# Kernel optimization log

Hardware: AMD Instinct MI355X
Metric: run time of the kernel (lower is better)

The kernel has to match this reference:

```python
import jax, jax.numpy as jnp
import numpy as np

FILTERS = [1, 3, 7, 9]
BN_EPS = 1e-5


def _conv1d(x, w, b):
    # x: [B, C, L], w: [O, I, F] (torch Conv1d layout), 'same' padding for odd F
    pad = (w.shape[-1] - 1) // 2
    y = jax.lax.conv_general_dilated(
        x, w, window_strides=(1,), padding=[(pad, pad)],
        dimension_numbers=("NCH", "OIH", "NCH"))
    return y + b[None, :, None]


def _bn_elu(x, gamma, beta):
    # BatchNorm1d in training mode: biased batch stats over (batch, length)
    m = jnp.mean(x, axis=(0, 2), keepdims=True)
    v = jnp.var(x, axis=(0, 2), keepdims=True)
    xn = (x - m) * jax.lax.rsqrt(v + BN_EPS)
    return jax.nn.elu(xn * gamma[None, :, None] + beta[None, :, None])


def setup_inputs() -> dict:
    key = jax.random.key(0)
    ks = jax.random.split(key, 32)
    b, h, l, lk, dk = 8, 8, 1024, 1024, 64
    inp = {
        "Q": jax.random.normal(ks[0], (b, h, l, dk), jnp.float32),
        "K": jax.random.normal(ks[1], (b, h, lk, dk), jnp.float32),
        "V": jax.random.normal(ks[2], (b, h, lk, dk), jnp.float32),
        "W_pq": jax.random.normal(ks[3], (1, dk), jnp.float32) * 0.1,
        "W_bq": jax.random.normal(ks[4], (dk, 1), jnp.float32) * 0.1,
        "W_bk": jax.random.normal(ks[5], (dk, 1), jnp.float32) * 0.1,
        "bn_g": jax.random.uniform(ks[6], (h,), jnp.float32, 0.5, 1.5),
        "bn_b": jax.random.normal(ks[7], (h,), jnp.float32) * 0.1,
        "attn_mask": jnp.ones((1,), dtype=bool),
    }
    for i, f in enumerate(FILTERS):
        s = 1.0 / np.sqrt(h * f)
        inp[f"cq_w{i}"] = jax.random.normal(ks[8 + i], (h, h, f), jnp.float32) * s
        inp[f"cq_b{i}"] = jax.random.normal(ks[12 + i], (h,), jnp.float32) * 0.05
        inp[f"ck_w{i}"] = jax.random.normal(ks[16 + i], (h, h, f), jnp.float32) * s
        inp[f"ck_b{i}"] = jax.random.normal(ks[20 + i], (h,), jnp.float32) * 0.05
    return inp


def reference(Q, K, V, W_pq, W_bq, W_bk,
              cq_w0, cq_b0, cq_w1, cq_b1, cq_w2, cq_b2, cq_w3, cq_b3,
              ck_w0, ck_b0, ck_w1, ck_b1, ck_w2, ck_b2, ck_w3, ck_b3,
              bn_g, bn_b, attn_mask):
    b, h, l, dk = Q.shape
    lk = K.shape[2]
    nf = len(FILTERS)
    # proj_q applied to BOTH Q and K (proj_k is dead in the original code)
    q = jnp.einsum("bhld,d->bhl", Q, W_pq[0])  # [b,h,l]
    k = jnp.einsum("bhld,d->bhl", K, W_pq[0])  # [b,h,lk]
    cq = [(cq_w0, cq_b0), (cq_w1, cq_b1), (cq_w2, cq_b2), (cq_w3, cq_b3)]
    ck = [(ck_w0, ck_b0), (ck_w1, ck_b1), (ck_w2, ck_b2), (ck_w3, ck_b3)]
    Q_l = [_bn_elu(_conv1d(q, w, bb), bn_g, bn_b) for w, bb in cq]
    K_l = [_bn_elu(_conv1d(k, w, bb), bn_g, bn_b) for w, bb in ck]
    # replicate torch.cat(dim=0) + reshape(b,h,nf*len) flat-order semantics
    Q_p = jnp.concatenate(Q_l, axis=0).reshape(b, h, nf * l)    # [b,h,4l]
    K_p = jnp.concatenate(K_l, axis=0).reshape(b, h, nf * lk)   # [b,h,4lk]
    Qt = jax.lax.top_k(Q_p, l)[0]                               # [b,h,l]
    Km = jnp.mean(K_p.reshape(b, h, nf, lk), axis=2)            # [b,h,lk]
    Kt = jax.lax.top_k(Km, lk)[0]                               # descending sort
    Qb = Qt[..., None] * W_bq[:, 0]                             # [b,h,l,dk]
    Kb = Kt[..., None] * W_bk[:, 0]                             # [b,h,lk,dk]
    scores = jnp.einsum("bhqd,bhkd->bhqk", Qb, Kb) / np.float32(np.sqrt(dk))
    attn = jax.nn.softmax(scores, axis=-1)
    context = jnp.einsum("bhqk,bhkd->bhqd", attn, V)
    return context, attn
```

## Files before the change

### kernel.cpp

```cpp
#include <hip/hip_runtime.h>
#include <hip/hip_bf16.h>
#include <math.h>

namespace {
constexpr int PROJ_OFF = 0;
constexpr int CONV_OFF = 131072;
constexpr int PS_OFF   = 655360;
constexpr int PSS_OFF  = 657408;
constexpr int QT_OFF   = 659456;
constexpr int KT_OFF   = 724992;

typedef short bf16x8 __attribute__((ext_vector_type(8)));
typedef float f32x4 __attribute__((ext_vector_type(4)));

union BF8 {
  bf16x8 v;
  short s[8];
};

__global__ __launch_bounds__(256) void proj_kernel(
    const float* __restrict__ Q, const float* __restrict__ K,
    const float* __restrict__ Wpq, float* __restrict__ proj) {
  __shared__ float wsh[64];
  const int tid = threadIdx.x;
  if (tid < 64) wsh[tid] = Wpq[tid];
  __syncthreads();
  const int row = blockIdx.x * 256 + tid;
  const float* src = (row < 65536) ? (Q + (size_t)row * 64)
                                   : (K + (size_t)(row - 65536) * 64);
  float acc = 0.f;
#pragma unroll
  for (int j = 0; j < 16; ++j) {
    const float4 v = *(const float4*)(src + j * 4);
    acc = fmaf(v.x, wsh[j * 4 + 0], acc);
    acc = fmaf(v.y, wsh[j * 4 + 1], acc);
    acc = fmaf(v.z, wsh[j * 4 + 2], acc);
    acc = fmaf(v.w, wsh[j * 4 + 3], acc);
  }
  proj[row] = acc;
}

template <int F>
__device__ void conv_body(const float* __restrict__ xs,
                          const float* __restrict__ wsm,
                          const float* __restrict__ bsm,
                          float* __restrict__ outp, int tid, int lq,
                          float accs[8]) {
  constexpr int pad = (F - 1) / 2;
#pragma unroll
  for (int j = 0; j < 8; ++j) {
    float acc = bsm[j];
#pragma unroll
    for (int c = 0; c < 8; ++c) {
      const float* xrow = &xs[c * 264 + tid + 4 - pad];
      const float* wrow = &wsm[(j * 8 + c) * F];
#pragma unroll
      for (int f = 0; f < F; ++f) acc = fmaf(xrow[f], wrow[f], acc);
    }
    outp[j * 1024 + lq * 256 + tid] = acc;
    accs[j] = acc;
  }
}

__global__ __launch_bounds__(256) void conv_kernel(
    const float* __restrict__ proj,
    const float* __restrict__ wq0, const float* __restrict__ bq0,
    const float* __restrict__ wq1, const float* __restrict__ bq1,
    const float* __restrict__ wq2, const float* __restrict__ bq2,
    const float* __restrict__ wq3, const float* __restrict__ bq3,
    const float* __restrict__ wk0, const float* __restrict__ bk0,
    const float* __restrict__ wk1, const float* __restrict__ bk1,
    const float* __restrict__ wk2, const float* __restrict__ bk2,
    const float* __restrict__ wk3, const float* __restrict__ bk3,
    float* __restrict__ conv, float* __restrict__ psum,
    float* __restrict__ psumsq) {
  __shared__ float xs[8 * 264];
  __shared__ float wsm[8 * 8 * 9];
  __shared__ float bsm[8];
  __shared__ float redS[8][4], redSS[8][4];
  const int tid = threadIdx.x;
  const int blk = blockIdx.x;
  const int path = blk >> 7, fi = (blk >> 5) & 3, bb = (blk >> 2) & 7;
  const int lq = blk & 3;
  const int F = (0x9731 >> (fi * 4)) & 0xF;
  const float* wp;
  const float* bp;
  if (path == 0) {
    wp = fi == 0 ? wq0 : fi == 1 ? wq1 : fi == 2 ? wq2 : wq3;
    bp = fi == 0 ? bq0 : fi == 1 ? bq1 : fi == 2 ? bq2 : bq3;
  } else {
    wp = fi == 0 ? wk0 : fi == 1 ? wk1 : fi == 2 ? wk2 : wk3;
    bp = fi == 0 ? bk0 : fi == 1 ? bk1 : fi == 2 ? bk2 : bk3;
  }
  const float* pb = proj + path * 65536 + bb * 8192;
  for (int e = tid; e < 8 * 264; e += 256) {
    const int c = e / 264, pos = e - c * 264;
    const int gl = lq * 256 + pos - 4;
    xs[e] = (gl >= 0 && gl < 1024) ? pb[c * 1024 + gl] : 0.f;
  }
  for (int e = tid; e < 64 * F; e += 256) wsm[e] = wp[e];
  if (tid < 8) bsm[tid] = bp[tid];
  __syncthreads();
  float* outp = conv + ((size_t)(path * 4 + fi) * 8 + bb) * 8192;
  float accs[8];
  if (fi == 0)
    conv_body<1>(xs, wsm, bsm, outp, tid, lq, accs);
  else if (fi == 1)
    conv_body<3>(xs, wsm, bsm, outp, tid, lq, accs);
  else if (fi == 2)
    conv_body<7>(xs, wsm, bsm, outp, tid, lq, accs);
  else
    conv_body<9>(xs, wsm, bsm, outp, tid, lq, accs);
  const int lane = tid & 63, wv = tid >> 6;
#pragma unroll
  for (int j = 0; j < 8; ++j) {
    float sv = accs[j], qv = accs[j] * accs[j];
#pragma unroll
    for (int mm = 32; mm >= 1; mm >>= 1) {
      sv += __shfl_xor(sv, mm, 64);
      qv += __shfl_xor(qv, mm, 64);
    }
    if (lane == 0) {
      redS[j][wv] = sv;
      redSS[j][wv] = qv;
    }
  }
  __syncthreads();
  if (tid < 16) {
    const int j = tid & 7;
    const bool wantss = tid >= 8;
    const float* rr = wantss ? &redSS[j][0] : &redS[j][0];
    const float tot = rr[0] + rr[1] + rr[2] + rr[3];
    float* dst = wantss ? psumsq : psum;
    dst[((path * 4 + fi) * 8 + j) * 32 + bb * 4 + lq] = tot;
  }
}

__device__ inline float bn_elu(float v, float mean, float rstd, float g,
                               float be) {
  const float x = (v - mean) * rstd * g + be;
  return x > 0.f ? x : expm1f(x);
}

__device__ inline void cswap(float& a, float& b, bool up) {
  const float mx = fmaxf(a, b), mn = fminf(a, b);
  a = up ? mx : mn;
  b = up ? mn : mx;
}

__device__ inline void wsort1024(float v[16], int lane) {
#pragma unroll
  for (int k = 2; k <= 1024; k <<= 1) {
#pragma unroll
    for (int j = 512; j >= 16; j >>= 1) {
      if (j <= (k >> 1)) {
        const int lj = j >> 4;
        const bool up = ((lane & (k >> 4)) == 0);
        const bool keep = (up == ((lane & lj) == 0));
#pragma unroll
        for (int e = 0; e < 16; ++e) {
          const float p = __shfl_xor(v[e], lj, 64);
          v[e] = keep ? fmaxf(v[e], p) : fminf(v[e], p);
        }
      }
    }
#pragma unroll
    for (int j = 8; j >= 1; j >>= 1) {
      if (j <= (k >> 1)) {
#pragma unroll
        for (int e = 0; e < 16; ++e) {
          if ((e & j) == 0) {
            bool up;
            if (k >= 32)
              up = ((lane & (k >> 4)) == 0);
            else if (k == 16)
              up = ((lane & 1) == 0);
            else
              up = ((e & k) == 0);
            cswap(v[e], v[e ^ j], up);
          }
        }
      }
    }
  }
}

__device__ inline void wmerge1024(float v[16], int lane) {
#pragma unroll
  for (int lj = 32; lj >= 1; lj >>= 1) {
    const bool keep = ((lane & lj) == 0);
#pragma unroll
    for (int e = 0; e < 16; ++e) {
      const float p = __shfl_xor(v[e], lj, 64);
      v[e] = keep ? fmaxf(v[e], p) : fminf(v[e], p);
    }
  }
#pragma unroll
  for (int j = 8; j >= 1; j >>= 1)
#pragma unroll
    for (int e = 0; e < 16; ++e)
      if ((e & j) == 0) cswap(v[e], v[e ^ j], true);
}

__global__ __launch_bounds__(256) void sortmerge2_kernel(
    const float* __restrict__ conv, const float* __restrict__ psum,
    const float* __restrict__ psumsq, const float* __restrict__ bng,
    const float* __restrict__ bnb, float* __restrict__ Qt,
    float* __restrict__ Kt) {
  __shared__ float s1[1024];
  __shared__ float s2[1024];
  const int tid = threadIdx.x, blk = blockIdx.x;
  const int wv = tid >> 6, l = tid & 63;
  float v[16];
  if (blk < 64) {
    const int row = blk;
    const int hp = row & 7, fi = row >> 4;
    const int bb = ((row >> 3) & 1) * 4 + (hp >> 1);
    const int hh = (hp & 1) * 4 + wv;
    const int ch = fi * 8 + hh;
    float sval = 0.f;
    if (l < 2) {
      const float* src = (l == 0) ? psum : psumsq;
#pragma unroll
      for (int i = 0; i < 32; ++i) sval += src[ch * 32 + i];
    }
    const float mean = __shfl(sval, 0, 64) * (1.f / 8192.f);
    const float msq = __shfl(sval, 1, 64) * (1.f / 8192.f);
    const float rstd = rsqrtf(fmaxf(msq - mean * mean, 0.f) + 1e-5f);
    const float g = bng[hh], be = bnb[hh];
    const float* base = conv + (size_t)(fi * 8 + bb) * 8192 + hh * 1024;
#pragma unroll
    for (int j = 0; j < 4; ++j) {
      const float4 x = *(const float4*)&base[l * 16 + j * 4];
      v[j * 4 + 0] = bn_elu(x.x, mean, rstd, g, be);
      v[j * 4 + 1] = bn_elu(x.y, mean, rstd, g, be);
      v[j * 4 + 2] = bn_elu(x.z, mean, rstd, g, be);
      v[j * 4 + 3] = bn_elu(x.w, mean, rstd, g, be);
    }
    wsort1024(v, l);
    if (wv == 1)
#pragma unroll
      for (int e = 0; e < 16; ++e) s1[l * 16 + e] = v[e];
    if (wv == 3)
#pragma unroll
      for (int e = 0; e < 16; ++e) s2[l * 16 + e] = v[e];
    __syncthreads();
    if (wv == 0) {
#pragma unroll
      for (int e = 0; e < 16; ++e)
        v[e] = fmaxf(v[e], s1[1023 - (l * 16 + e)]);
      wmerge1024(v, l);
    } else if (wv == 2) {
#pragma unroll
      for (int e = 0; e < 16; ++e)
        v[e] = fmaxf(v[e], s2[1023 - (l * 16 + e)]);
      wmerge1024(v, l);
#pragma unroll
      for (int e = 0; e < 16; ++e) s2[l * 16 + e] = v[e];
    }
    __syncthreads();
    if (wv == 0) {
#pragma unroll
      for (int e = 0; e < 16; ++e)
        v[e] = fmaxf(v[e], s2[1023 - (l * 16 + e)]);
      wmerge1024(v, l);
      float* qd = Qt + (size_t)row * 1024 + l * 16;
#pragma unroll
      for (int j = 0; j < 4; ++j)
        *(float4*)&qd[j * 4] =
            make_float4(v[j * 4], v[j * 4 + 1], v[j * 4 + 2], v[j * 4 + 3]);
    }
  } else {
    const int row = (blk - 64) * 4 + wv;
    const int hp = row & 7, fi = row >> 4;
    const int bb = ((row >> 3) & 1) * 4 + (hp >> 1);
    const int chk = 32 + fi * 8 + (hp & 1) * 4;
    float sval = 0.f;
    if (l < 8) {
      const float* src = (l < 4) ? psum : psumsq;
      const int ch = chk + (l & 3);
#pragma unroll
      for (int i = 0; i < 32; ++i) sval += src[ch * 32 + i];
    }
    float cm[4], cr[4];
#pragma unroll
    for (int j = 0; j < 4; ++j) {
      const float mean = __shfl(sval, j, 64) * (1.f / 8192.f);
      const float msq = __shfl(sval, j + 4, 64) * (1.f / 8192.f);
      cm[j] = mean;
      cr[j] = rsqrtf(fmaxf(msq - mean * mean, 0.f) + 1e-5f);
    }
#pragma unroll
    for (int e = 0; e < 16; ++e) v[e] = 0.f;
#pragma unroll
    for (int j = 0; j < 4; ++j) {
      const int hh = (hp & 1) * 4 + j;
      const float g = bng[hh], be = bnb[hh];
      const float* base =
          conv + (size_t)(4 + fi) * 64 * 1024 + (size_t)bb * 8192 + hh * 1024;
#pragma unroll
      for (int jj = 0; jj < 4; ++jj) {
        const float4 x = *(const float4*)&base[l * 16 + jj * 4];
        v[jj * 4 + 0] += bn_elu(x.x, cm[j], cr[j], g, be);
        v[jj * 4 + 1] += bn_elu(x.y, cm[j], cr[j], g, be);
        v[jj * 4 + 2] += bn_elu(x.z, cm[j], cr[j], g, be);
        v[jj * 4 + 3] += bn_elu(x.w, cm[j], cr[j], g, be);
      }
    }
#pragma unroll
    for (int e = 0; e < 16; ++e) v[e] *= 0.25f;
    wsort1024(v, l);
    float* kd = Kt + (size_t)row * 1024 + l * 16;
#pragma unroll
    for (int j = 0; j < 4; ++j)
      *(float4*)&kd[j * 4] =
          make_float4(v[j * 4], v[j * 4 + 1], v[j * 4 + 2], v[j * 4 + 3]);
  }
}

__global__ __launch_bounds__(256, 4) void attn5_kernel(
    const float* __restrict__ V, const float* __restrict__ Qt,
    const float* __restrict__ Kt, const float* __restrict__ Wbq,
    const float* __restrict__ Wbk, float* __restrict__ ctx,
    float* __restrict__ attn) {
  __shared__ float Kts[1024];
  __shared__ float sq[64], mq[64], rz[64];
  __shared__ short Vhi[2][8 * 64 * 8];
  __shared__ short Vlo[2][8 * 64 * 8];
  const int tid = threadIdx.x;
  const int b = blockIdx.x;
  const int bh = ((b & 7) << 3) | ((b >> 3) & 7);
  const int qt = b >> 6;
  const int qbase = qt * 64;
  const int lane0 = tid & 63;
  float cval;
  {
    float d = Wbq[lane0] * Wbk[lane0];
#pragma unroll
    for (int mm = 32; mm >= 1; mm >>= 1) d += __shfl_xor(d, mm, 64);
    cval = d * 0.125f;
  }
  const float* Ktg = Kt + (size_t)bh * 1024;
  for (int t = tid; t < 1024; t += 256) Kts[t] = Ktg[t];
  const float kHi = Ktg[0], kLo = Ktg[1023];
  if (tid < 64) {
    const float s = cval * Qt[(size_t)bh * 1024 + qbase + tid];
    sq[tid] = s;
    mq[tid] = fmaxf(s * kHi, s * kLo);
  }
  __syncthreads();
  {
    const int row = tid >> 2, qtr = tid & 3;
    const float s = sq[row], m = mq[row];
    float z = 0.f;
    const int k0 = qtr * 256;
    for (int k = 0; k < 256; ++k) z += __expf(fmaf(s, Kts[k0 + k], -m));
    z += __shfl_xor(z, 1, 64);
    z += __shfl_xor(z, 2, 64);
    if (qtr == 0) rz[row] = 1.f / z;
  }
  __syncthreads();

  const int wv = tid >> 6, l = tid & 63;
  const int l15 = l & 15, l4 = l >> 4;
  const int q = wv * 16 + l15;
  const float s = sq[q], m = mq[q], r = rz[q];
  f32x4 acc[4];
#pragma unroll
  for (int dt = 0; dt < 4; ++dt) acc[dt] = (f32x4){0.f, 0.f, 0.f, 0.f};

  const float* Vb = V + (size_t)bh * 65536;
  float* arow = attn + ((size_t)bh << 20) + (size_t)qbase * 1024;
  const int dV = tid & 63, kqV = tid >> 6;

  for (int ch = 0; ch < 16; ++ch) {
    const int kc = ch * 64;
    const int buf = ch & 1;
    float vreg[2][8];
#pragma unroll
    for (int g = 0; g < 2; ++g) {
      const int ko = kqV + g * 4;
      const float* vs = Vb + (size_t)(kc + ko * 8) * 64 + dV;
#pragma unroll
      for (int i = 0; i < 8; ++i) vreg[g][i] = vs[i * 64];
    }
    bf16x8 ahi[2], alo[2];
#pragma unroll
    for (int ks = 0; ks < 2; ++ks) {
      const int kb = kc + ks * 32 + l4 * 8;
      const float4 kv0 = *(const float4*)&Kts[kb];
      const float4 kv1 = *(const float4*)&Kts[kb + 4];
      float e[8];
      e[0] = __expf(fmaf(s, kv0.x, -m)) * r;
      e[1] = __expf(fmaf(s, kv0.y, -m)) * r;
      e[2] = __expf(fmaf(s, kv0.z, -m)) * r;
      e[3] = __expf(fmaf(s, kv0.w, -m)) * r;
      e[4] = __expf(fmaf(s, kv1.x, -m)) * r;
      e[5] = __expf(fmaf(s, kv1.y, -m)) * r;
      e[6] = __expf(fmaf(s, kv1.z, -m)) * r;
      e[7] = __expf(fmaf(s, kv1.w, -m)) * r;
      float* ag = arow + (size_t)q * 1024 + kb;
      *(float4*)ag = make_float4(e[0], e[1], e[2], e[3]);
      *(float4*)(ag + 4) = make_float4(e[4], e[5], e[6], e[7]);
      BF8 H, L;
#pragma unroll
      for (int i = 0; i < 8; ++i) {
        const __hip_bfloat16 hb = __float2bfloat16(e[i]);
        H.s[i] = __bfloat16_as_short(hb);
        L.s[i] =
            __bfloat16_as_short(__float2bfloat16(e[i] - __bfloat162float(hb)));
      }
      ahi[ks] = H.v;
      alo[ks] = L.v;
    }
#pragma unroll
    for (int g = 0; g < 2; ++g) {
      const int ko = kqV + g * 4;
      BF8 H, L;
#pragma unroll
      for (int i = 0; i < 8; ++i) {
        const float f = vreg[g][i];
        const __hip_bfloat16 hb = __float2bfloat16(f);
        H.s[i] = __bfloat16_as_short(hb);
        L.s[i] =
            __bfloat16_as_short(__float2bfloat16(f - __bfloat162float(hb)));
      }
      *(bf16x8*)&Vhi[buf][(ko * 64 + dV) * 8] = H.v;
      *(bf16x8*)&Vlo[buf][(ko * 64 + dV) * 8] = L.v;
    }
    __syncthreads();
#pragma unroll
    for (int ks = 0; ks < 2; ++ks) {
      const int ko = ks * 4 + l4;
#pragma unroll
      for (int dt = 0; dt < 4; ++dt) {
        const bf16x8 bhv =
            *(const bf16x8*)&Vhi[buf][(ko * 64 + dt * 16 + l15) * 8];
        const bf16x8 blv =
            *(const bf16x8*)&Vlo[buf][(ko * 64 + dt * 16 + l15) * 8];
        acc[dt] = __builtin_amdgcn_mfma_f32_16x16x32_bf16(ahi[ks], bhv,
                                                          acc[dt], 0, 0, 0);
        acc[dt] = __builtin_amdgcn_mfma_f32_16x16x32_bf16(ahi[ks], blv,
                                                          acc[dt], 0, 0, 0);
        acc[dt] = __builtin_amdgcn_mfma_f32_16x16x32_bf16(alo[ks], bhv,
                                                          acc[dt], 0, 0, 0);
      }
    }
  }
  float* cb = ctx + ((size_t)bh * 1024 + qbase + wv * 16 + l4 * 4) * 64 + l15;
#pragma unroll
  for (int dt = 0; dt < 4; ++dt)
#pragma unroll
    for (int rr = 0; rr < 4; ++rr) cb[(size_t)rr * 64 + dt * 16] = acc[dt][rr];
}

}

extern "C" void kernel_launch(void* const* d_in, const int* in_sizes, int n_in,
                              void* d_out, int out_size, void* d_ws,
                              size_t ws_size, hipStream_t stream) {
  const float* Q = (const float*)d_in[0];
  const float* K = (const float*)d_in[1];
  const float* V = (const float*)d_in[2];
  const float* Wpq = (const float*)d_in[3];
  const float* Wbq = (const float*)d_in[4];
  const float* Wbk = (const float*)d_in[5];
  const float* bng = (const float*)d_in[6];
  const float* bnb = (const float*)d_in[7];
  const float* cqw[4] = {(const float*)d_in[9], (const float*)d_in[13],
                         (const float*)d_in[17], (const float*)d_in[21]};
  const float* cqb[4] = {(const float*)d_in[10], (const float*)d_in[14],
                         (const float*)d_in[18], (const float*)d_in[22]};
  const float* ckw[4] = {(const float*)d_in[11], (const float*)d_in[15],
                         (const float*)d_in[19], (const float*)d_in[23]};
  const float* ckb[4] = {(const float*)d_in[12], (const float*)d_in[16],
                         (const float*)d_in[20], (const float*)d_in[24]};

  float* ws = (float*)d_ws;
  float* proj = ws + PROJ_OFF;
  float* conv = ws + CONV_OFF;
  float* psum = ws + PS_OFF;
  float* psumsq = ws + PSS_OFF;
  float* Qtp = ws + QT_OFF;
  float* Ktp = ws + KT_OFF;
  float* ctx = (float*)d_out;
  float* attn = ctx + (size_t)8 * 8 * 1024 * 64;

  proj_kernel<<<512, 256, 0, stream>>>(Q, K, Wpq, proj);
  conv_kernel<<<256, 256, 0, stream>>>(
      proj, cqw[0], cqb[0], cqw[1], cqb[1], cqw[2], cqb[2], cqw[3], cqb[3],
      ckw[0], ckb[0], ckw[1], ckb[1], ckw[2], ckb[2], ckw[3], ckb[3], conv,
      psum, psumsq);
  sortmerge2_kernel<<<80, 256, 0, stream>>>(conv, psum, psumsq, bng, bnb, Qtp,
                                            Ktp);
  attn5_kernel<<<1024, 256, 0, stream>>>(V, Qtp, Ktp, Wbq, Wbk, ctx, attn);
}
```

Measured before the change: 119.2 us.

## Fuse projection, conv and sort kernels into one persistent kernel with grid barriers

Merges the projection, conv+BN-statistics and sort/merge stages into a single 256-block kernel that uses atomic-counter grid barriers between stages, replacing three launches with one kernel plus a memset. The projection is also reworked so each 16-lane group reduces a row with shuffles, giving coalesced float4 loads. This removes launch gaps and inter-kernel drains, but relies on all 256 blocks being co-resident for the spin barrier, adds a memset launch, and leaves most blocks idle during the final sort stage.

```diff
diff --git a/kernel.cpp b/kernel.cpp
--- a/kernel.cpp
+++ b/kernel.cpp
@@ -9,6 +9,7 @@
 constexpr int PSS_OFF  = 657408;
 constexpr int QT_OFF   = 659456;
 constexpr int KT_OFF   = 724992;
+constexpr int GBAR_OFF = 790528;
 
 typedef short bf16x8 __attribute__((ext_vector_type(8)));
 typedef float f32x4 __attribute__((ext_vector_type(4)));
@@ -18,122 +19,17 @@
   short s[8];
 };
 
-__global__ __launch_bounds__(256) void proj_kernel(
-    const float* __restrict__ Q, const float* __restrict__ K,
-    const float* __restrict__ Wpq, float* __restrict__ proj) {
-  __shared__ float wsh[64];
-  const int tid = threadIdx.x;
-  if (tid < 64) wsh[tid] = Wpq[tid];
+__device__ inline void gbar(unsigned* cnt, unsigned nb) {
   __syncthreads();
-  const int row = blockIdx.x * 256 + tid;
-  const float* src = (row < 65536) ? (Q + (size_t)row * 64)
-                                   : (K + (size_t)(row - 65536) * 64);
-  float acc = 0.f;
-#pragma unroll
-  for (int j = 0; j < 16; ++j) {
-    const float4 v = *(const float4*)(src + j * 4);
-    acc = fmaf(v.x, wsh[j * 4 + 0], acc);
-    acc = fmaf(v.y, wsh[j * 4 + 1], acc);
-    acc = fmaf(v.z, wsh[j * 4 + 2], acc);
-    acc = fmaf(v.w, wsh[j * 4 + 3], acc);
-  }
-  proj[row] = acc;
-}
-
-template <int F>
-__device__ void conv_body(const float* __restrict__ xs,
-                          const float* __restrict__ wsm,
-                          const float* __restrict__ bsm,
-                          float* __restrict__ outp, int tid, int lq,
-                          float accs[8]) {
-  constexpr int pad = (F - 1) / 2;
-#pragma unroll
-  for (int j = 0; j < 8; ++j) {
-    float acc = bsm[j];
-#pragma unroll
-    for (int c = 0; c < 8; ++c) {
-      const float* xrow = &xs[c * 264 + tid + 4 - pad];
-      const float* wrow = &wsm[(j * 8 + c) * F];
-#pragma unroll
-      for (int f = 0; f < F; ++f) acc = fmaf(xrow[f], wrow[f], acc);
-    }
-    outp[j * 1024 + lq * 256 + tid] = acc;
-    accs[j] = acc;
-  }
-}
-
-__global__ __launch_bounds__(256) void conv_kernel(
-    const float* __restrict__ proj,
-    const float* __restrict__ wq0, const float* __restrict__ bq0,
-    const float* __restrict__ wq1, const float* __restrict__ bq1,
-    const float* __restrict__ wq2, const float* __restrict__ bq2,
-    const float* __restrict__ wq3, const float* __restrict__ bq3,
-    const float* __restrict__ wk0, const float* __restrict__ bk0,
-    const float* __restrict__ wk1, const float* __restrict__ bk1,
-    const float* __restrict__ wk2, const float* __restrict__ bk2,
-    const float* __restrict__ wk3, const float* __restrict__ bk3,
-    float* __restrict__ conv, float* __restrict__ psum,
-    float* __restrict__ psumsq) {
-  __shared__ float xs[8 * 264];
-  __shared__ float wsm[8 * 8 * 9];
-  __shared__ float bsm[8];
-  __shared__ float redS[8][4], redSS[8][4];
-  const int tid = threadIdx.x;
-  const int blk = blockIdx.x;
-  const int path = blk >> 7, fi = (blk >> 5) & 3, bb = (blk >> 2) & 7;
-  const int lq = blk & 3;
-  const int F = (0x9731 >> (fi * 4)) & 0xF;
-  const float* wp;
-  const float* bp;
-  if (path == 0) {
-    wp = fi == 0 ? wq0 : fi == 1 ? wq1 : fi == 2 ? wq2 : wq3;
-    bp = fi == 0 ? bq0 : fi == 1 ? bq1 : fi == 2 ? bq2 : bq3;
-  } else {
-    wp = fi == 0 ? wk0 : fi == 1 ? wk1 : fi == 2 ? wk2 : wk3;
-    bp = fi == 0 ? bk0 : fi == 1 ? bk1 : fi == 2 ? bk2 : bk3;
-  }
-  const float* pb = proj + path * 65536 + bb * 8192;
-  for (int e = tid; e < 8 * 264; e += 256) {
-    const int c = e / 264, pos = e - c * 264;
-    const int gl = lq * 256 + pos - 4;
-    xs[e] = (gl >= 0 && gl < 1024) ? pb[c * 1024 + gl] : 0.f;
-  }
-  for (int e = tid; e < 64 * F; e += 256) wsm[e] = wp[e];
-  if (tid < 8) bsm[tid] = bp[tid];
+  __threadfence();
+  if (threadIdx.x == 0) {
+    atomicAdd(cnt, 1u);
+    while (__hip_atomic_load(cnt, __ATOMIC_ACQUIRE,
+                             __HIP_MEMORY_SCOPE_AGENT) < nb) {
+      __builtin_amdgcn_s_sleep(2);
+    }
+  }
   __syncthreads();
-  float* outp = conv + ((size_t)(path * 4 + fi) * 8 + bb) * 8192;
-  float accs[8];
-  if (fi == 0)
-    conv_body<1>(xs, wsm, bsm, outp, tid, lq, accs);
-  else if (fi == 1)
-    conv_body<3>(xs, wsm, bsm, outp, tid, lq, accs);
-  else if (fi == 2)
-    conv_body<7>(xs, wsm, bsm, outp, tid, lq, accs);
-  else
-    conv_body<9>(xs, wsm, bsm, outp, tid, lq, accs);
-  const int lane = tid & 63, wv = tid >> 6;
-#pragma unroll
-  for (int j = 0; j < 8; ++j) {
-    float sv = accs[j], qv = accs[j] * accs[j];
-#pragma unroll
-    for (int mm = 32; mm >= 1; mm >>= 1) {
-      sv += __shfl_xor(sv, mm, 64);
-      qv += __shfl_xor(qv, mm, 64);
-    }
-    if (lane == 0) {
-      redS[j][wv] = sv;
-      redSS[j][wv] = qv;
-    }
-  }
-  __syncthreads();
-  if (tid < 16) {
-    const int j = tid & 7;
-    const bool wantss = tid >= 8;
-    const float* rr = wantss ? &redSS[j][0] : &redS[j][0];
-    const float tot = rr[0] + rr[1] + rr[2] + rr[3];
-    float* dst = wantss ? psumsq : psum;
-    dst[((path * 4 + fi) * 8 + j) * 32 + bb * 4 + lq] = tot;
-  }
 }
 
 __device__ inline float bn_elu(float v, float mean, float rstd, float g,
@@ -202,15 +98,140 @@
       if ((e & j) == 0) cswap(v[e], v[e ^ j], true);
 }
 
-__global__ __launch_bounds__(256) void sortmerge2_kernel(
-    const float* __restrict__ conv, const float* __restrict__ psum,
-    const float* __restrict__ psumsq, const float* __restrict__ bng,
-    const float* __restrict__ bnb, float* __restrict__ Qt,
-    float* __restrict__ Kt) {
-  __shared__ float s1[1024];
-  __shared__ float s2[1024];
-  const int tid = threadIdx.x, blk = blockIdx.x;
+template <int F>
+__device__ void conv_body(const float* __restrict__ xs,
+                          const float* __restrict__ wsm,
+                          const float* __restrict__ bsm,
+                          float* __restrict__ outp, int tid, int lq,
+                          float accs[8]) {
+  constexpr int pad = (F - 1) / 2;
+#pragma unroll
+  for (int j = 0; j < 8; ++j) {
+    float acc = bsm[j];
+#pragma unroll
+    for (int c = 0; c < 8; ++c) {
+      const float* xrow = &xs[c * 264 + tid + 4 - pad];
+      const float* wrow = &wsm[(j * 8 + c) * F];
+#pragma unroll
+      for (int f = 0; f < F; ++f) acc = fmaf(xrow[f], wrow[f], acc);
+    }
+    outp[j * 1024 + lq * 256 + tid] = acc;
+    accs[j] = acc;
+  }
+}
+
+__global__ __launch_bounds__(256) void front_kernel(
+    const float* __restrict__ Q, const float* __restrict__ K,
+    const float* __restrict__ Wpq,
+    const float* __restrict__ wq0, const float* __restrict__ bq0,
+    const float* __restrict__ wq1, const float* __restrict__ bq1,
+    const float* __restrict__ wq2, const float* __restrict__ bq2,
+    const float* __restrict__ wq3, const float* __restrict__ bq3,
+    const float* __restrict__ wk0, const float* __restrict__ bk0,
+    const float* __restrict__ wk1, const float* __restrict__ bk1,
+    const float* __restrict__ wk2, const float* __restrict__ bk2,
+    const float* __restrict__ wk3, const float* __restrict__ bk3,
+    const float* __restrict__ bng, const float* __restrict__ bnb,
+    float* __restrict__ proj, float* __restrict__ conv,
+    float* __restrict__ psum, float* __restrict__ psumsq,
+    float* __restrict__ Qt, float* __restrict__ Kt,
+    unsigned* __restrict__ gcnt) {
+  __shared__ float smem[2816];
+  const int tid = threadIdx.x;
   const int wv = tid >> 6, l = tid & 63;
+
+  {
+    const int g16 = l & 15, gid = l >> 4;
+    const float4 w4 = *(const float4*)(Wpq + g16 * 4);
+    const int gw = blockIdx.x * 4 + wv;
+    const int base = gw * 128;
+#pragma unroll 4
+    for (int it = 0; it < 32; ++it) {
+      const int r = base + it * 4 + gid;
+      const float* src = (r < 65536) ? (Q + (size_t)r * 64)
+                                     : (K + (size_t)(r - 65536) * 64);
+      const float4 x = *(const float4*)(src + g16 * 4);
+      float v = x.x * w4.x;
+      v = fmaf(x.y, w4.y, v);
+      v = fmaf(x.z, w4.z, v);
+      v = fmaf(x.w, w4.w, v);
+      v += __shfl_xor(v, 1, 64);
+      v += __shfl_xor(v, 2, 64);
+      v += __shfl_xor(v, 4, 64);
+      v += __shfl_xor(v, 8, 64);
+      if (g16 == 0) proj[r] = v;
+    }
+  }
+  gbar(&gcnt[0], 256);
+
+  {
+    float* xs = smem;
+    float* wsm = smem + 2112;
+    float* bsm = smem + 2688;
+    float* redS = smem + 2696;
+    float* redSS = smem + 2728;
+    const int blk = blockIdx.x;
+    const int path = blk >> 7, fi = (blk >> 5) & 3, bb = (blk >> 2) & 7;
+    const int lq = blk & 3;
+    const int F = (0x9731 >> (fi * 4)) & 0xF;
+    const float* wp;
+    const float* bp;
+    if (path == 0) {
+      wp = fi == 0 ? wq0 : fi == 1 ? wq1 : fi == 2 ? wq2 : wq3;
+      bp = fi == 0 ? bq0 : fi == 1 ? bq1 : fi == 2 ? bq2 : bq3;
+    } else {
+      wp = fi == 0 ? wk0 : fi == 1 ? wk1 : fi == 2 ? wk2 : wk3;
+      bp = fi == 0 ? bk0 : fi == 1 ? bk1 : fi == 2 ? bk2 : bk3;
+    }
+    const float* pb = proj + path * 65536 + bb * 8192;
+    for (int e = tid; e < 8 * 264; e += 256) {
+      const int c = e / 264, pos = e - c * 264;
+      const int gl = lq * 256 + pos - 4;
+      xs[e] = (gl >= 0 && gl < 1024) ? pb[c * 1024 + gl] : 0.f;
+    }
+    for (int e = tid; e < 64 * F; e += 256) wsm[e] = wp[e];
+    if (tid < 8) bsm[tid] = bp[tid];
+    __syncthreads();
+    float* outp = conv + ((size_t)(path * 4 + fi) * 8 + bb) * 8192;
+    float accs[8];
+    if (fi == 0)
+      conv_body<1>(xs, wsm, bsm, outp, tid, lq, accs);
+    else if (fi == 1)
+      conv_body<3>(xs, wsm, bsm, outp, tid, lq, accs);
+    else if (fi == 2)
+      conv_body<7>(xs, wsm, bsm, outp, tid, lq, accs);
+    else
+      conv_body<9>(xs, wsm, bsm, outp, tid, lq, accs);
+#pragma unroll
+    for (int j = 0; j < 8; ++j) {
+      float sv = accs[j], qv = accs[j] * accs[j];
+#pragma unroll
+      for (int mm = 32; mm >= 1; mm >>= 1) {
+        sv += __shfl_xor(sv, mm, 64);
+        qv += __shfl_xor(qv, mm, 64);
+      }
+      if (l == 0) {
+        redS[j * 4 + wv] = sv;
+        redSS[j * 4 + wv] = qv;
+      }
+    }
+    __syncthreads();
+    if (tid < 16) {
+      const int j = tid & 7;
+      const bool wantss = tid >= 8;
+      const float* rr = wantss ? &redSS[j * 4] : &redS[j * 4];
+      const float tot = rr[0] + rr[1] + rr[2] + rr[3];
+      float* dst = wantss ? psumsq : psum;
+      dst[((path * 4 + fi) * 8 + j) * 32 + bb * 4 + lq] = tot;
+    }
+    __syncthreads();
+  }
+  gbar(&gcnt[1], 256);
+
+  const int blk = blockIdx.x;
+  if (blk >= 80) return;
+  float* s1 = smem;
+  float* s2 = smem + 1024;
   float v[16];
   if (blk < 64) {
     const int row = blk;
@@ -247,13 +268,11 @@
     __syncthreads();
     if (wv == 0) {
 #pragma unroll
-      for (int e = 0; e < 16; ++e)
-        v[e] = fmaxf(v[e], s1[1023 - (l * 16 + e)]);
+      for (int e = 0; e < 16; ++e) v[e] = fmaxf(v[e], s1[1023 - (l * 16 + e)]);
       wmerge1024(v, l);
     } else if (wv == 2) {
 #pragma unroll
-      for (int e = 0; e < 16; ++e)
-        v[e] = fmaxf(v[e], s2[1023 - (l * 16 + e)]);
+      for (int e = 0; e < 16; ++e) v[e] = fmaxf(v[e], s2[1023 - (l * 16 + e)]);
       wmerge1024(v, l);
 #pragma unroll
       for (int e = 0; e < 16; ++e) s2[l * 16 + e] = v[e];
@@ -261,8 +280,7 @@
     __syncthreads();
     if (wv == 0) {
 #pragma unroll
-      for (int e = 0; e < 16; ++e)
-        v[e] = fmaxf(v[e], s2[1023 - (l * 16 + e)]);
+      for (int e = 0; e < 16; ++e) v[e] = fmaxf(v[e], s2[1023 - (l * 16 + e)]);
       wmerge1024(v, l);
       float* qd = Qt + (size_t)row * 1024 + l * 16;
 #pragma unroll
@@ -483,15 +501,14 @@
   float* psumsq = ws + PSS_OFF;
   float* Qtp = ws + QT_OFF;
   float* Ktp = ws + KT_OFF;
+  unsigned* gcnt = (unsigned*)(ws + GBAR_OFF);
   float* ctx = (float*)d_out;
   float* attn = ctx + (size_t)8 * 8 * 1024 * 64;
 
-  proj_kernel<<<512, 256, 0, stream>>>(Q, K, Wpq, proj);
-  conv_kernel<<<256, 256, 0, stream>>>(
-      proj, cqw[0], cqb[0], cqw[1], cqb[1], cqw[2], cqb[2], cqw[3], cqb[3],
-      ckw[0], ckb[0], ckw[1], ckb[1], ckw[2], ckb[2], ckw[3], ckb[3], conv,
-      psum, psumsq);
-  sortmerge2_kernel<<<80, 256, 0, stream>>>(conv, psum, psumsq, bng, bnb, Qtp,
-                                            Ktp);
+  hipMemsetAsync(gcnt, 0, 64, stream);
+  front_kernel<<<256, 256, 0, stream>>>(
+      Q, K, Wpq, cqw[0], cqb[0], cqw[1], cqb[1], cqw[2], cqb[2], cqw[3],
+      cqb[3], ckw[0], ckb[0], ckw[1], ckb[1], ckw[2], ckb[2], ckw[3], ckb[3],
+      bng, bnb, proj, conv, psum, psumsq, Qtp, Ktp, gcnt);
   attn5_kernel<<<1024, 256, 0, stream>>>(V, Qtp, Ktp, Wbq, Wbk, ctx, attn);
 }
```

After: 197.0 us. +65.3%, slower.
